# Kernel tuning notes

Hardware: AMD Instinct MI355X
Metric: run time of the kernel (lower is better)

The kernel has to match this reference:

```python
import jax, jax.numpy as jnp
import numpy as np

B, L, H = 1, 2048, 2048          # batch, seq_len, hidden_size
E, N, K, R = 4096, 16, 4, 128    # intermediate, ssm_state, conv_kernel, dt_rank


def setup_inputs() -> dict:
    key = jax.random.key(0)
    ks = jax.random.split(key, 8)
    s = 0.02
    inp = {
        "hidden_states": jax.random.normal(ks[0], (B, L, H), jnp.float32),
        "in_proj_w": jax.random.normal(ks[1], (2 * E, H), jnp.float32) * s,
        "conv_w": jax.random.normal(ks[2], (E, 1, K), jnp.float32) * s,
        "conv_b": jax.random.normal(ks[3], (E,), jnp.float32) * s,
        "x_proj_w": jax.random.normal(ks[4], (R + 2 * N, E), jnp.float32) * s,
        "dt_proj_w": jax.random.normal(ks[5], (E, R), jnp.float32) * s,
        "dt_proj_b": jax.random.normal(ks[6], (E,), jnp.float32) * s,
        "A_log": jnp.broadcast_to(jnp.log(jnp.arange(1, N + 1, dtype=jnp.float32))[None, :], (E, N)).copy(),
        "D": jnp.ones((E,), jnp.float32),
        "out_proj_w": jax.random.normal(ks[7], (H, E), jnp.float32) * s,
    }
    return inp


def _mamba_mixer(hidden_states, in_proj_w, conv_w, conv_b, x_proj_w,
                 dt_proj_w, dt_proj_b, A_log, D, out_proj_w):
    # in_proj -> [B, L, 2E], split into hidden / gate
    proj = jnp.einsum('blh,eh->ble', hidden_states, in_proj_w)
    h, gate = jnp.split(proj, 2, axis=-1)            # each [B, L, E]

    # depthwise causal conv1d over time, padding K-1 on the left
    h_c = h.transpose(0, 2, 1)                       # [B, E, L]
    h_c = jax.lax.conv_general_dilated(
        h_c, conv_w, window_strides=(1,), padding=[(K - 1, 0)],
        feature_group_count=E, dimension_numbers=('NCH', 'OIH', 'NCH'))
    h_c = h_c + conv_b[None, :, None]
    h = jax.nn.silu(h_c).transpose(0, 2, 1)          # [B, L, E]

    # x_proj -> dt, B, C (input-dependent SSM params)
    ssm = jnp.einsum('ble,pe->blp', h, x_proj_w)     # [B, L, R+2N]
    dt, Bp, Cp = jnp.split(ssm, [R, R + N], axis=-1)
    dt = jax.nn.softplus(jnp.einsum('blr,er->ble', dt, dt_proj_w) + dt_proj_b)  # [B,L,E]

    A = -jnp.exp(A_log)                              # [E, N]
    dA = jnp.exp(dt[..., None] * A)                  # [B, L, E, N]
    dBu = (dt * h)[..., None] * Bp[:, :, None, :]    # [B, L, E, N]

    # selective scan: s_t = dA_t * s_{t-1} + dBu_t
    def step(s, xs):
        dA_t, dBu_t = xs
        s = s * dA_t + dBu_t
        return s, s

    s0 = jnp.zeros((h.shape[0], E, N), h.dtype)
    _, states = jax.lax.scan(step, s0, (dA.transpose(1, 0, 2, 3), dBu.transpose(1, 0, 2, 3)))
    # states: [L, B, E, N]
    y = jnp.einsum('lben,bln->ble', states, Cp)      # [B, L, E]
    y = y + h * D                                    # skip via D
    y = y * jax.nn.silu(gate)                        # gated output
    return jnp.einsum('ble,he->blh', y, out_proj_w)  # [B, L, H]


def reference(hidden_states, in_proj_w, conv_w, conv_b, x_proj_w,
              dt_proj_w, dt_proj_b, A_log, D, out_proj_w):
    return _mamba_mixer(hidden_states, in_proj_w, conv_w, conv_b, x_proj_w,
                        dt_proj_w, dt_proj_b, A_log, D, out_proj_w)
```

## Files before the change

kernel.cpp:

```cpp
#include <hip/hip_runtime.h>

#define LL 2048
#define HH 2048
#define EE 4096
#define NS 16
#define RR 128
#define CT 32
#define NC (LL / CT)
#define BM 128
#define BN 128
#define BK 64

typedef __bf16 bf16x8 __attribute__((ext_vector_type(8)));
typedef float f32x4 __attribute__((ext_vector_type(4)));

__device__ __forceinline__ unsigned short f2bf(float f) {
  union { float f; unsigned int u; } v; v.f = f;
  unsigned int r = v.u + 0x7fffu + ((v.u >> 16) & 1u);
  return (unsigned short)(r >> 16);
}

__device__ __forceinline__ float bf2f(unsigned short u) {
  union { unsigned int i; float f; } v;
  v.i = ((unsigned int)u) << 16;
  return v.f;
}

__device__ __forceinline__ float softplus_fast(float x) {
  if (x > 20.0f) return x;
  float e = __builtin_amdgcn_exp2f(1.44269504f * x);
  return 0.69314718f * __builtin_amdgcn_logf(1.0f + e);
}

__device__ __forceinline__ void async_cp16(const unsigned short* g,
                                           unsigned short* l) {
  __builtin_amdgcn_global_load_lds(
      (const __attribute__((address_space(1))) unsigned int*)g,
      (__attribute__((address_space(3))) unsigned int*)l, 16, 0, 0);
}

#define P_C0 (LL * HH / 4)
#define P_C1 (P_C0 + 2 * EE * HH / 4)
#define P_C2 (P_C1 + 160 * EE / 4)
#define P_C3 (P_C2 + EE * RR / 4)
#define P_C4 (P_C3 + HH * EE / 4)
#define P_C5 (P_C4 + LL * 160 / 4)
#define P_C6 (P_C5 + LL * HH / 4)

__global__ __launch_bounds__(256) void prep_k(
    const float* __restrict__ hs, unsigned short* __restrict__ hsb,
    const float* __restrict__ w1, unsigned short* __restrict__ w1b,
    const float* __restrict__ xw, unsigned short* __restrict__ xwb,
    const float* __restrict__ dtw, unsigned short* __restrict__ dtwb,
    const float* __restrict__ ow, unsigned short* __restrict__ owb,
    float* __restrict__ ssm, float* __restrict__ out) {
  int i = blockIdx.x * 256 + threadIdx.x;
  const float* src = nullptr;
  unsigned short* dst = nullptr;
  int k = 0;
  if (i < P_C0)      { src = hs;  dst = hsb;  k = i; }
  else if (i < P_C1) { src = w1;  dst = w1b;  k = i - P_C0; }
  else if (i < P_C2) { src = xw;  dst = xwb;  k = i - P_C1; }
  else if (i < P_C3) { src = dtw; dst = dtwb; k = i - P_C2; }
  else if (i < P_C4) { src = ow;  dst = owb;  k = i - P_C3; }
  else if (i < P_C5) {
    float4 z; z.x = z.y = z.z = z.w = 0.0f;
    reinterpret_cast<float4*>(ssm)[i - P_C4] = z;
    return;
  } else {
    float4 z; z.x = z.y = z.z = z.w = 0.0f;
    reinterpret_cast<float4*>(out)[i - P_C5] = z;
    return;
  }
  float4 v = reinterpret_cast<const float4*>(src)[k];
  ushort4 o;
  o.x = f2bf(v.x); o.y = f2bf(v.y); o.z = f2bf(v.z); o.w = f2bf(v.w);
  reinterpret_cast<ushort4*>(dst)[k] = o;
}

template <int EPI>
__global__ __launch_bounds__(512, 2) void gemm256(
    const unsigned short* __restrict__ A,
    const unsigned short* __restrict__ B,
    float* __restrict__ C,
    int M, int N, int K, int tilesM, int splitk,
    float* __restrict__ auxF, unsigned short* __restrict__ auxB) {
  __shared__ __align__(16) unsigned short As[2][16384];
  __shared__ __align__(16) unsigned short Bs[2][16384];

  int bid = blockIdx.x;
  int tnInner = bid & 7;
  int rest = bid >> 3;
  int tm = rest % tilesM;
  int tn = (rest / tilesM) * 8 + tnInner;

  int Kslice = K / splitk;
  int k_begin = blockIdx.y * Kslice;
  int NT = Kslice / 64;

  int tid = threadIdx.x;
  int lane = tid & 63;
  int wave = tid >> 6;
  int wm = wave >> 2;
  int wn = wave & 3;
  int m16 = lane & 15, quad = lane >> 4;

  const unsigned short* Ab = A + (size_t)tm * 256 * K;
  const unsigned short* Bb = B + (size_t)tn * 256 * K;

  int rowS = tid >> 3;
  int gcbS = (tid & 7) ^ (rowS & 7);
  int ldsWB = (tid & ~63) * 8;

  int sw = m16 & 7;
  int coff0 = (quad ^ sw) << 3;
  int coff1 = ((4 + quad) ^ sw) << 3;
  int aoff = (wm * 128 + m16) * 64;
  int boff = (wn * 64 + m16) * 64;

  f32x4 acc[8][4];
#pragma unroll
  for (int i = 0; i < 8; ++i)
#pragma unroll
    for (int j = 0; j < 4; ++j)
#pragma unroll
      for (int t = 0; t < 4; ++t) acc[i][j][t] = 0.0f;

  auto stageA = [&](int bufb, int t, int h) {
    int kt = k_begin + t * 64;
    unsigned short* dst = &As[bufb][0];
#pragma unroll
    for (int c = 2 * h; c < 2 * h + 2; ++c)
      async_cp16(Ab + (size_t)(c * 64 + rowS) * K + kt + gcbS * 8,
                 dst + c * 4096 + ldsWB);
  };
  auto stageB = [&](int bufb, int t, int h) {
    int kt = k_begin + t * 64;
    unsigned short* dst = &Bs[bufb][0];
#pragma unroll
    for (int c = 2 * h; c < 2 * h + 2; ++c)
      async_cp16(Bb + (size_t)(c * 64 + rowS) * K + kt + gcbS * 8,
                 dst + c * 4096 + ldsWB);
  };

  stageA(0, 0, 0); stageA(0, 0, 1);
  stageB(0, 0, 0); stageB(0, 0, 1);
  stageB(1, 1, 0); stageB(1, 1, 1);
  stageA(1, 1, 0);
  asm volatile("s_waitcnt vmcnt(6)" ::: "memory");
  __builtin_amdgcn_s_barrier();

  bf16x8 a[4][2], b0[2][2], b1[2][2];

  for (int t0 = 0; t0 < NT; t0 += 2) {
    int t1 = t0 + 1;
    bool notLast = (t0 + 2 < NT);
    unsigned short* A0 = &As[0][0];
    unsigned short* B0 = &Bs[0][0];
    unsigned short* A1 = &As[1][0];
    unsigned short* B1 = &Bs[1][0];

#pragma unroll
    for (int i = 0; i < 4; ++i) {
      a[i][0] = *reinterpret_cast<const bf16x8*>(&A0[aoff + i * 1024 + coff0]);
      a[i][1] = *reinterpret_cast<const bf16x8*>(&A0[aoff + i * 1024 + coff1]);
    }
#pragma unroll
    for (int j = 0; j < 2; ++j) {
      b0[j][0] = *reinterpret_cast<const bf16x8*>(&B0[boff + j * 1024 + coff0]);
      b0[j][1] = *reinterpret_cast<const bf16x8*>(&B0[boff + j * 1024 + coff1]);
    }
    stageA(1, t1, 1);
    __builtin_amdgcn_s_barrier();
    asm volatile("s_waitcnt lgkmcnt(0)" ::: "memory");
    __builtin_amdgcn_sched_barrier(0);
    __builtin_amdgcn_s_setprio(1);
#pragma unroll
    for (int kk = 0; kk < 2; ++kk)
#pragma unroll
      for (int i = 0; i < 4; ++i)
#pragma unroll
        for (int j = 0; j < 2; ++j)
          acc[i][j] = __builtin_amdgcn_mfma_f32_16x16x32_bf16(
              a[i][kk], b0[j][kk], acc[i][j], 0, 0, 0);
    __builtin_amdgcn_s_setprio(0);
    __builtin_amdgcn_s_barrier();

#pragma unroll
    for (int j = 0; j < 2; ++j) {
      b1[j][0] = *reinterpret_cast<const bf16x8*>(&B0[boff + (2 + j) * 1024 + coff0]);
      b1[j][1] = *reinterpret_cast<const bf16x8*>(&B0[boff + (2 + j) * 1024 + coff1]);
    }
    __builtin_amdgcn_s_barrier();
    asm volatile("s_waitcnt lgkmcnt(0)" ::: "memory");
    __builtin_amdgcn_sched_barrier(0);
    __builtin_amdgcn_s_setprio(1);
#pragma unroll
    for (int kk = 0; kk < 2; ++kk)
#pragma unroll
      for (int i = 0; i < 4; ++i)
#pragma unroll
        for (int j = 0; j < 2; ++j)
          acc[i][2 + j] = __builtin_amdgcn_mfma_f32_16x16x32_bf16(
              a[i][kk], b1[j][kk], acc[i][2 + j], 0, 0, 0);
    __builtin_amdgcn_s_setprio(0);
    __builtin_amdgcn_s_barrier();

#pragma unroll
    for (int i = 0; i < 4; ++i) {
      a[i][0] = *reinterpret_cast<const bf16x8*>(&A0[aoff + (4 + i) * 1024 + coff0]);
      a[i][1] = *reinterpret_cast<const bf16x8*>(&A0[aoff + (4 + i) * 1024 + coff1]);
    }
    if (notLast) stageB(0, t0 + 2, 0);
    __builtin_amdgcn_s_barrier();
    asm volatile("s_waitcnt lgkmcnt(0)" ::: "memory");
    __builtin_amdgcn_sched_barrier(0);
    __builtin_amdgcn_s_setprio(1);
#pragma unroll
    for (int kk = 0; kk < 2; ++kk)
#pragma unroll
      for (int i = 0; i < 4; ++i)
#pragma unroll
        for (int j = 0; j < 2; ++j)
          acc[4 + i][2 + j] = __builtin_amdgcn_mfma_f32_16x16x32_bf16(
              a[i][kk], b1[j][kk], acc[4 + i][2 + j], 0, 0, 0);
    __builtin_amdgcn_s_setprio(0);
    __builtin_amdgcn_s_barrier();

    if (notLast) stageB(0, t0 + 2, 1);
    __builtin_amdgcn_s_setprio(1);
#pragma unroll
    for (int kk = 0; kk < 2; ++kk)
#pragma unroll
      for (int i = 0; i < 4; ++i)
#pragma unroll
        for (int j = 0; j < 2; ++j)
          acc[4 + i][j] = __builtin_amdgcn_mfma_f32_16x16x32_bf16(
              a[i][kk], b0[j][kk], acc[4 + i][j], 0, 0, 0);
    __builtin_amdgcn_s_setprio(0);
    if (notLast) {
      asm volatile("s_waitcnt vmcnt(4)" ::: "memory");
    } else {
      asm volatile("s_waitcnt vmcnt(0)" ::: "memory");
    }
    __builtin_amdgcn_s_barrier();

#pragma unroll
    for (int i = 0; i < 4; ++i) {
      a[i][0] = *reinterpret_cast<const bf16x8*>(&A1[aoff + i * 1024 + coff0]);
      a[i][1] = *reinterpret_cast<const bf16x8*>(&A1[aoff + i * 1024 + coff1]);
    }
#pragma unroll
    for (int j = 0; j < 2; ++j) {
      b0[j][0] = *reinterpret_cast<const bf16x8*>(&B1[boff + j * 1024 + coff0]);
      b0[j][1] = *reinterpret_cast<const bf16x8*>(&B1[boff + j * 1024 + coff1]);
    }
    if (notLast) stageA(0, t0 + 2, 0);
    __builtin_amdgcn_s_barrier();
    asm volatile("s_waitcnt lgkmcnt(0)" ::: "memory");
    __builtin_amdgcn_sched_barrier(0);
    __builtin_amdgcn_s_setprio(1);
#pragma unroll
    for (int kk = 0; kk < 2; ++kk)
#pragma unroll
      for (int i = 0; i < 4; ++i)
#pragma unroll
        for (int j = 0; j < 2; ++j)
          acc[i][j] = __builtin_amdgcn_mfma_f32_16x16x32_bf16(
              a[i][kk], b0[j][kk], acc[i][j], 0, 0, 0);
    __builtin_amdgcn_s_setprio(0);
    __builtin_amdgcn_s_barrier();

#pragma unroll
    for (int j = 0; j < 2; ++j) {
      b1[j][0] = *reinterpret_cast<const bf16x8*>(&B1[boff + (2 + j) * 1024 + coff0]);
      b1[j][1] = *reinterpret_cast<const bf16x8*>(&B1[boff + (2 + j) * 1024 + coff1]);
    }
    if (notLast) stageA(0, t0 + 2, 1);
    __builtin_amdgcn_s_barrier();
    asm volatile("s_waitcnt lgkmcnt(0)" ::: "memory");
    __builtin_amdgcn_sched_barrier(0);
    __builtin_amdgcn_s_setprio(1);
#pragma unroll
    for (int kk = 0; kk < 2; ++kk)
#pragma unroll
      for (int i = 0; i < 4; ++i)
#pragma unroll
        for (int j = 0; j < 2; ++j)
          acc[i][2 + j] = __builtin_amdgcn_mfma_f32_16x16x32_bf16(
              a[i][kk], b1[j][kk], acc[i][2 + j], 0, 0, 0);
    __builtin_amdgcn_s_setprio(0);
    __builtin_amdgcn_s_barrier();

#pragma unroll
    for (int i = 0; i < 4; ++i) {
      a[i][0] = *reinterpret_cast<const bf16x8*>(&A1[aoff + (4 + i) * 1024 + coff0]);
      a[i][1] = *reinterpret_cast<const bf16x8*>(&A1[aoff + (4 + i) * 1024 + coff1]);
    }
    if (notLast) stageB(1, t1 + 2, 0);
    __builtin_amdgcn_s_barrier();
    asm volatile("s_waitcnt lgkmcnt(0)" ::: "memory");
    __builtin_amdgcn_sched_barrier(0);
    __builtin_amdgcn_s_setprio(1);
#pragma unroll
    for (int kk = 0; kk < 2; ++kk)
#pragma unroll
      for (int i = 0; i < 4; ++i)
#pragma unroll
        for (int j = 0; j < 2; ++j)
          acc[4 + i][2 + j] = __builtin_amdgcn_mfma_f32_16x16x32_bf16(
              a[i][kk], b1[j][kk], acc[4 + i][2 + j], 0, 0, 0);
    __builtin_amdgcn_s_setprio(0);
    __builtin_amdgcn_s_barrier();

    if (notLast) { stageB(1, t1 + 2, 1); stageA(1, t1 + 2, 0); }
    __builtin_amdgcn_s_setprio(1);
#pragma unroll
    for (int kk = 0; kk < 2; ++kk)
#pragma unroll
      for (int i = 0; i < 4; ++i)
#pragma unroll
        for (int j = 0; j < 2; ++j)
          acc[4 + i][j] = __builtin_amdgcn_mfma_f32_16x16x32_bf16(
              a[i][kk], b0[j][kk], acc[4 + i][j], 0, 0, 0);
    __builtin_amdgcn_s_setprio(0);
    if (notLast) {
      asm volatile("s_waitcnt vmcnt(6)" ::: "memory");
    }
    __builtin_amdgcn_s_barrier();
  }

  int rowB = tm * 256 + wm * 128;
  int colB = tn * 256 + wn * 64;
  if constexpr (EPI == 1) {
#pragma unroll
    for (int mi = 0; mi < 8; ++mi)
#pragma unroll
      for (int nj = 0; nj < 4; ++nj) {
        int col = colB + nj * 16 + m16;
        int row0 = rowB + mi * 16 + quad * 4;
#pragma unroll
        for (int t4 = 0; t4 < 4; ++t4)
          atomicAdd(&C[(size_t)(row0 + t4) * N + col], acc[mi][nj][t4]);
      }
  } else {
    if (colB < EE) {
#pragma unroll
      for (int mi = 0; mi < 8; ++mi)
#pragma unroll
        for (int nj = 0; nj < 4; ++nj) {
          int col = colB + nj * 16 + m16;
          int row0 = rowB + mi * 16 + quad * 4;
#pragma unroll
          for (int t4 = 0; t4 < 4; ++t4)
            auxF[(size_t)(row0 + t4) * EE + col] = acc[mi][nj][t4];
        }
    } else {
#pragma unroll
      for (int mi = 0; mi < 8; ++mi)
#pragma unroll
        for (int nj = 0; nj < 4; ++nj) {
          int cg = colB + nj * 16 + m16 - EE;
          int row0 = rowB + mi * 16 + quad * 4;
#pragma unroll
          for (int t4 = 0; t4 < 4; ++t4) {
            float v = acc[mi][nj][t4];
            float s = v / (1.0f + __expf(-v));
            auxB[(size_t)(row0 + t4) * EE + cg] = f2bf(s);
          }
        }
    }
  }
}

template <int EPI>
__global__ __launch_bounds__(256) void gemm_lds_t(
    const unsigned short* __restrict__ A,
    const unsigned short* __restrict__ B,
    float* __restrict__ C,
    int M, int N, int K, int tilesM, int splitk,
    const float* __restrict__ bias, float* __restrict__ auxF,
    unsigned short* __restrict__ auxB) {
  __shared__ __align__(16) unsigned short As[BM * BK];
  __shared__ __align__(16) unsigned short Bs[BN * BK];

  int bid = blockIdx.x;
  int tnInner = bid & 7;
  int rest = bid >> 3;
  int tm = rest % tilesM;
  int tnOuter = rest / tilesM;
  int tn = tnOuter * 8 + tnInner;

  int Kslice = K / splitk;
  int k_begin = blockIdx.y * Kslice;
  int k_end = k_begin + Kslice;

  int tid = threadIdx.x;
  int lane = tid & 63;
  int wave = tid >> 6;
  int wm = wave & 1, wn = wave >> 1;
  int m16 = lane & 15, quad = lane >> 4;

  const unsigned short* Ab = A + (size_t)tm * BM * K;
  const unsigned short* Bb = B + (size_t)tn * BN * K;

  int srow[4], sgcb[4];
#pragma unroll
  for (int it = 0; it < 4; ++it) {
    int blk = it * 256 + tid;
    srow[it] = blk >> 3;
    sgcb[it] = (blk & 7) ^ (srow[it] & 7);
  }
  int ldsbase = (tid & ~63) * 8;

  f32x4 acc[4][4];
#pragma unroll
  for (int i = 0; i < 4; ++i)
#pragma unroll
    for (int j = 0; j < 4; ++j)
#pragma unroll
      for (int t = 0; t < 4; ++t) acc[i][j][t] = 0.0f;

  for (int k0 = k_begin; k0 < k_end; k0 += BK) {
    __syncthreads();
#pragma unroll
    for (int it = 0; it < 4; ++it)
      async_cp16(Ab + (size_t)srow[it] * K + k0 + sgcb[it] * 8,
                 &As[it * 2048 + ldsbase]);
#pragma unroll
    for (int it = 0; it < 4; ++it)
      async_cp16(Bb + (size_t)srow[it] * K + k0 + sgcb[it] * 8,
                 &Bs[it * 2048 + ldsbase]);
    __syncthreads();
#pragma unroll
    for (int kk = 0; kk < 2; ++kk) {
      bf16x8 a[4], b[4];
#pragma unroll
      for (int i = 0; i < 4; ++i) {
        int rr = wm * 64 + i * 16 + m16;
        int cb = (kk << 2) + quad;
        a[i] = *reinterpret_cast<const bf16x8*>(
            &As[rr * BK + ((cb ^ (rr & 7)) << 3)]);
      }
#pragma unroll
      for (int j = 0; j < 4; ++j) {
        int rr = wn * 64 + j * 16 + m16;
        int cb = (kk << 2) + quad;
        b[j] = *reinterpret_cast<const bf16x8*>(
            &Bs[rr * BK + ((cb ^ (rr & 7)) << 3)]);
      }
#pragma unroll
      for (int i = 0; i < 4; ++i)
#pragma unroll
        for (int j = 0; j < 4; ++j)
          acc[i][j] =
              __builtin_amdgcn_mfma_f32_16x16x32_bf16(a[i], b[j], acc[i][j], 0, 0, 0);
    }
  }

  int rowB = tm * BM + wm * 64;
  int colB = tn * BN + wn * 64;
  if constexpr (EPI == 1) {
#pragma unroll
    for (int i = 0; i < 4; ++i)
#pragma unroll
      for (int j = 0; j < 4; ++j) {
        int col = colB + j * 16 + m16;
        int row0 = rowB + i * 16 + quad * 4;
#pragma unroll
        for (int t = 0; t < 4; ++t)
          atomicAdd(&C[(size_t)(row0 + t) * N + col], acc[i][j][t]);
      }
  } else {
#pragma unroll
    for (int i = 0; i < 4; ++i)
#pragma unroll
      for (int j = 0; j < 4; ++j) {
        int col = colB + j * 16 + m16;
        float bv = bias[col];
        int row0 = rowB + i * 16 + quad * 4;
#pragma unroll
        for (int t = 0; t < 4; ++t) {
          float x = acc[i][j][t] + bv;
          auxB[(size_t)(row0 + t) * EE + col] = f2bf(softplus_fast(x));
        }
      }
  }
}

__global__ __launch_bounds__(256) void gemm_bt(
    const unsigned short* __restrict__ A,
    const unsigned short* __restrict__ B,
    float* __restrict__ C,
    int M, int N, int K, int tilesN, int splitk) {
  int bid = blockIdx.x;
  int groupSize = 8 * tilesN;
  int g = bid / groupSize, r = bid % groupSize;
  int tm = g * 8 + (r & 7);
  int tn = r >> 3;

  int Kslice = K / splitk;
  int k_begin = blockIdx.y * Kslice;
  int k_end = k_begin + Kslice;

  int tid = threadIdx.x;
  int wave = tid >> 6, lane = tid & 63;
  int wm = wave & 1, wn = wave >> 1;
  int m16 = lane & 15, quad = lane >> 4;
  int rowBase = tm * 64 + wm * 32;
  int colBase = tn * 128 + wn * 64;

  const unsigned short* a0p = A + (size_t)(rowBase + m16) * K + quad * 8;
  const unsigned short* a1p = A + (size_t)(rowBase + 16 + m16) * K + quad * 8;
  const unsigned short* bp[4];
  bool bok[4];
#pragma unroll
  for (int j = 0; j < 4; ++j) {
    int col = colBase + j * 16 + m16;
    bok[j] = (col < N);
    bp[j] = B + (size_t)(bok[j] ? col : 0) * K + quad * 8;
  }

  f32x4 acc[2][4];
#pragma unroll
  for (int i = 0; i < 2; ++i)
#pragma unroll
    for (int j = 0; j < 4; ++j)
#pragma unroll
      for (int t = 0; t < 4; ++t) acc[i][j][t] = 0.0f;

  bf16x8 zero8;
#pragma unroll
  for (int t = 0; t < 8; ++t) zero8[t] = (__bf16)0.0f;

  for (int k = k_begin; k < k_end; k += 32) {
    bf16x8 a0 = *reinterpret_cast<const bf16x8*>(a0p + k);
    bf16x8 a1 = *reinterpret_cast<const bf16x8*>(a1p + k);
    bf16x8 b[4];
#pragma unroll
    for (int j = 0; j < 4; ++j)
      b[j] = bok[j] ? *reinterpret_cast<const bf16x8*>(bp[j] + k) : zero8;
#pragma unroll
    for (int j = 0; j < 4; ++j) {
      acc[0][j] = __builtin_amdgcn_mfma_f32_16x16x32_bf16(a0, b[j], acc[0][j], 0, 0, 0);
      acc[1][j] = __builtin_amdgcn_mfma_f32_16x16x32_bf16(a1, b[j], acc[1][j], 0, 0, 0);
    }
  }

#pragma unroll
  for (int i = 0; i < 2; ++i)
#pragma unroll
    for (int j = 0; j < 4; ++j) {
      int col = colBase + j * 16 + m16;
      if (col >= N) continue;
      int row0 = rowBase + i * 16 + quad * 4;
      if (splitk == 1) {
#pragma unroll
        for (int t = 0; t < 4; ++t)
          C[(size_t)(row0 + t) * N + col] = acc[i][j][t];
      } else {
#pragma unroll
        for (int t = 0; t < 4; ++t)
          atomicAdd(&C[(size_t)(row0 + t) * N + col], acc[i][j][t]);
      }
    }
}

__global__ __launch_bounds__(256) void conv_silu_k(
    const float* __restrict__ projh, const float* __restrict__ cw,
    const float* __restrict__ cb, unsigned short* __restrict__ hb) {
  int e = blockIdx.x * 256 + threadIdx.x;
  int l0 = blockIdx.y * 16;
  float w0 = cw[e * 4 + 0], w1 = cw[e * 4 + 1];
  float w2 = cw[e * 4 + 2], w3 = cw[e * 4 + 3];
  float bias = cb[e];
  float xm3 = (l0 >= 3) ? projh[(size_t)(l0 - 3) * EE + e] : 0.0f;
  float xm2 = (l0 >= 2) ? projh[(size_t)(l0 - 2) * EE + e] : 0.0f;
  float xm1 = (l0 >= 1) ? projh[(size_t)(l0 - 1) * EE + e] : 0.0f;
#pragma unroll
  for (int t = 0; t < 16; ++t) {
    int l = l0 + t;
    float x0 = projh[(size_t)l * EE + e];
    float acc = bias + w0 * xm3 + w1 * xm2 + w2 * xm1 + w3 * x0;
    float s = acc / (1.0f + __expf(-acc));
    hb[(size_t)l * EE + e] = f2bf(s);
    xm3 = xm2; xm2 = xm1; xm1 = x0;
  }
}

__global__ void dtcast_k(const float* __restrict__ ssm,
                         unsigned short* __restrict__ dtin, int n) {
  int i = blockIdx.x * blockDim.x + threadIdx.x;
  if (i >= n) return;
  int l = i >> 7, r = i & 127;
  dtin[i] = f2bf(ssm[l * 160 + r]);
}

__global__ __launch_bounds__(256) void scan_partA(
    const unsigned short* __restrict__ dtb, const unsigned short* __restrict__ hb,
    const float* __restrict__ ssm, const float* __restrict__ A_log,
    float* __restrict__ P, float* __restrict__ S) {
  int e = blockIdx.y * 256 + threadIdx.x;
  int c = blockIdx.x;
  float Aa[16];
#pragma unroll
  for (int q = 0; q < 4; ++q) {
    float4 a = reinterpret_cast<const float4*>(&A_log[(size_t)e * NS])[q];
    Aa[q * 4 + 0] = -__expf(a.x) * 1.44269504f;
    Aa[q * 4 + 1] = -__expf(a.y) * 1.44269504f;
    Aa[q * 4 + 2] = -__expf(a.z) * 1.44269504f;
    Aa[q * 4 + 3] = -__expf(a.w) * 1.44269504f;
  }
  float s[16], p[16];
#pragma unroll
  for (int n = 0; n < 16; ++n) { s[n] = 0.0f; p[n] = 1.0f; }
  int l0 = c * CT;
#pragma unroll 2
  for (int t = 0; t < CT; ++t) {
    int l = l0 + t;
    size_t o = (size_t)l * EE + e;
    float dtv = bf2f(dtb[o]);
    float hv = bf2f(hb[o]);
    float Bv[16];
#pragma unroll
    for (int q = 0; q < 4; ++q)
      *reinterpret_cast<float4*>(&Bv[q * 4]) =
          reinterpret_cast<const float4*>(&ssm[(size_t)l * 160 + 128])[q];
    float z = dtv * hv;
#pragma unroll
    for (int n = 0; n < 16; ++n) {
      float dA = __builtin_amdgcn_exp2f(dtv * Aa[n]);
      s[n] = s[n] * dA + z * Bv[n];
      p[n] *= dA;
    }
  }
  size_t base = ((size_t)c * EE + e) * NS;
#pragma unroll
  for (int q = 0; q < 4; ++q) {
    reinterpret_cast<float4*>(&P[base])[q] = *reinterpret_cast<float4*>(&p[q * 4]);
    reinterpret_cast<float4*>(&S[base])[q] = *reinterpret_cast<float4*>(&s[q * 4]);
  }
}

__global__ __launch_bounds__(256) void scan_chunkB(
    const float* __restrict__ P, float* __restrict__ S) {
  int gidx = blockIdx.x * 256 + threadIdx.x;
  float s = 0.0f;
  float pv = P[gidx], sv = S[gidx];
  for (int c = 0; c < NC; ++c) {
    float pn = 0.0f, sn = 0.0f;
    if (c + 1 < NC) {
      size_t i2 = (size_t)(c + 1) * (EE * NS) + gidx;
      pn = P[i2];
      sn = S[i2];
    }
    float s_next = s * pv + sv;
    S[(size_t)c * (EE * NS) + gidx] = s;
    s = s_next;
    pv = pn; sv = sn;
  }
}

__global__ __launch_bounds__(256) void scan_partC(
    const unsigned short* __restrict__ dtb, const unsigned short* __restrict__ hb,
    const float* __restrict__ ssm, const float* __restrict__ A_log,
    const float* __restrict__ Dp, const unsigned short* __restrict__ sg,
    const float* __restrict__ Sinit, unsigned short* __restrict__ yb) {
  int e = blockIdx.y * 256 + threadIdx.x;
  int c = blockIdx.x;
  float Aa[16];
#pragma unroll
  for (int q = 0; q < 4; ++q) {
    float4 a = reinterpret_cast<const float4*>(&A_log[(size_t)e * NS])[q];
    Aa[q * 4 + 0] = -__expf(a.x) * 1.44269504f;
    Aa[q * 4 + 1] = -__expf(a.y) * 1.44269504f;
    Aa[q * 4 + 2] = -__expf(a.z) * 1.44269504f;
    Aa[q * 4 + 3] = -__expf(a.w) * 1.44269504f;
  }
  float Dv = Dp[e];
  float s[16];
  size_t base = ((size_t)c * EE + e) * NS;
#pragma unroll
  for (int q = 0; q < 4; ++q)
    *reinterpret_cast<float4*>(&s[q * 4]) =
        reinterpret_cast<const float4*>(&Sinit[base])[q];
  int l0 = c * CT;
#pragma unroll 2
  for (int t = 0; t < CT; ++t) {
    int l = l0 + t;
    size_t o = (size_t)l * EE + e;
    float dtv = bf2f(dtb[o]);
    float hv = bf2f(hb[o]);
    float Bv[16], Cv[16];
#pragma unroll
    for (int q = 0; q < 4; ++q) {
      *reinterpret_cast<float4*>(&Bv[q * 4]) =
          reinterpret_cast<const float4*>(&ssm[(size_t)l * 160 + 128])[q];
      *reinterpret_cast<float4*>(&Cv[q * 4]) =
          reinterpret_cast<const float4*>(&ssm[(size_t)l * 160 + 144])[q];
    }
    float z = dtv * hv;
    float y = 0.0f;
#pragma unroll
    for (int n = 0; n < 16; ++n) {
      float dA = __builtin_amdgcn_exp2f(dtv * Aa[n]);
      s[n] = s[n] * dA + z * Bv[n];
      y += s[n] * Cv[n];
    }
    float gv = bf2f(sg[o]);
    float yv = (y + hv * Dv) * gv;
    yb[o] = f2bf(yv);
  }
}

extern "C" void kernel_launch(void* const* d_in, const int* in_sizes, int n_in,
                              void* d_out, int out_size, void* d_ws, size_t ws_size,
                              hipStream_t stream) {
  const float* hs   = (const float*)d_in[0];
  const float* w1   = (const float*)d_in[1];
  const float* cw   = (const float*)d_in[2];
  const float* cb   = (const float*)d_in[3];
  const float* xw   = (const float*)d_in[4];
  const float* dtw  = (const float*)d_in[5];
  const float* dtb  = (const float*)d_in[6];
  const float* Alog = (const float*)d_in[7];
  const float* Dp   = (const float*)d_in[8];
  const float* ow   = (const float*)d_in[9];
  float* out = (float*)d_out;

  char* ws = (char*)d_ws;
  size_t off = 0;
  auto alloc = [&](size_t b) {
    char* p = ws + off;
    off += (b + 255) & ~(size_t)255;
    return p;
  };
  float* projh = (float*)alloc((size_t)LL * EE * 4);
  unsigned short* sg  = (unsigned short*)alloc((size_t)LL * EE * 2);
  unsigned short* hb  = (unsigned short*)alloc((size_t)LL * EE * 2);
  unsigned short* dtb_buf = (unsigned short*)alloc((size_t)LL * EE * 2);
  unsigned short* w1b = (unsigned short*)alloc((size_t)2 * EE * HH * 2);
  unsigned short* hsb = (unsigned short*)alloc((size_t)LL * HH * 2);
  unsigned short* yb  = (unsigned short*)alloc((size_t)LL * EE * 2);
  unsigned short* owb = (unsigned short*)alloc((size_t)HH * EE * 2);
  unsigned short* xwb = (unsigned short*)alloc((size_t)160 * EE * 2);
  float* ssm = (float*)alloc((size_t)LL * 160 * 4);
  unsigned short* dtin = (unsigned short*)alloc((size_t)LL * RR * 2);
  unsigned short* dtwb = (unsigned short*)alloc((size_t)EE * RR * 2);
  float* Pbuf = (float*)alloc((size_t)NC * EE * NS * 4);
  float* Sbuf = (float*)alloc((size_t)NC * EE * NS * 4);

  prep_k<<<P_C6 / 256, 256, 0, stream>>>(hs, hsb, w1, w1b, xw, xwb, dtw, dtwb,
                                         ow, owb, ssm, out);

  {
    int tilesM = LL / 256;
    int tilesN = (2 * EE) / 256;
    gemm256<2><<<dim3(tilesM * tilesN, 1), 512, 0, stream>>>(
        hsb, w1b, nullptr, LL, 2 * EE, HH, tilesM, 1, projh, sg);
  }
  conv_silu_k<<<dim3(EE / 256, LL / 16), 256, 0, stream>>>(projh, cw, cb, hb);
  {
    int tilesN = (160 + 127) / 128, tilesM = LL / 64;
    gemm_bt<<<dim3(tilesM * tilesN, 8), 256, 0, stream>>>(
        hb, xwb, ssm, LL, 160, EE, tilesN, 8);
  }
  dtcast_k<<<(LL * RR + 255) / 256, 256, 0, stream>>>(ssm, dtin, LL * RR);
  {
    int tilesN = EE / BN, tilesM = LL / BM;
    gemm_lds_t<4><<<dim3(tilesM * tilesN, 1), 256, 0, stream>>>(
        dtin, dtwb, nullptr, LL, EE, RR, tilesM, 1, dtb, nullptr, dtb_buf);
  }
  scan_partA<<<dim3(NC, EE / 256), 256, 0, stream>>>(dtb_buf, hb, ssm, Alog,
                                                     Pbuf, Sbuf);
  scan_chunkB<<<EE * NS / 256, 256, 0, stream>>>(Pbuf, Sbuf);
  scan_partC<<<dim3(NC, EE / 256), 256, 0, stream>>>(dtb_buf, hb, ssm, Alog, Dp,
                                                     sg, Sbuf, yb);
  {
    int tilesN = HH / BN, tilesM = LL / BM;
    gemm_lds_t<1><<<dim3(tilesM * tilesN, 2), 256, 0, stream>>>(
        yb, owb, out, LL, HH, EE, tilesM, 2, nullptr, nullptr, nullptr);
  }
}
```

Baseline: 416.2 us.

## Replace split-K out_proj GEMM with double-buffered async-LDS 128x128 kernel

New measurement: 393.0 us. -5.6%, faster.

```diff
diff --git a/kernel.cpp b/kernel.cpp
--- a/kernel.cpp
+++ b/kernel.cpp
@@ -45,7 +45,6 @@
 #define P_C3 (P_C2 + EE * RR / 4)
 #define P_C4 (P_C3 + HH * EE / 4)
 #define P_C5 (P_C4 + LL * 160 / 4)
-#define P_C6 (P_C5 + LL * HH / 4)
 
 __global__ __launch_bounds__(256) void prep_k(
     const float* __restrict__ hs, unsigned short* __restrict__ hsb,
@@ -53,7 +52,7 @@
     const float* __restrict__ xw, unsigned short* __restrict__ xwb,
     const float* __restrict__ dtw, unsigned short* __restrict__ dtwb,
     const float* __restrict__ ow, unsigned short* __restrict__ owb,
-    float* __restrict__ ssm, float* __restrict__ out) {
+    float* __restrict__ ssm) {
   int i = blockIdx.x * 256 + threadIdx.x;
   const float* src = nullptr;
   unsigned short* dst = nullptr;
@@ -63,13 +62,9 @@
   else if (i < P_C2) { src = xw;  dst = xwb;  k = i - P_C1; }
   else if (i < P_C3) { src = dtw; dst = dtwb; k = i - P_C2; }
   else if (i < P_C4) { src = ow;  dst = owb;  k = i - P_C3; }
-  else if (i < P_C5) {
+  else {
     float4 z; z.x = z.y = z.z = z.w = 0.0f;
     reinterpret_cast<float4*>(ssm)[i - P_C4] = z;
-    return;
-  } else {
-    float4 z; z.x = z.y = z.z = z.w = 0.0f;
-    reinterpret_cast<float4*>(out)[i - P_C5] = z;
     return;
   }
   float4 v = reinterpret_cast<const float4*>(src)[k];
@@ -371,6 +366,268 @@
         }
     }
   }
+}
+
+__global__ __launch_bounds__(256, 2) void gemm128p(
+    const unsigned short* __restrict__ A,
+    const unsigned short* __restrict__ B,
+    float* __restrict__ C,
+    int M, int N, int K, int tilesM) {
+  __shared__ __align__(16) unsigned short As[2][8192];
+  __shared__ __align__(16) unsigned short Bs[2][8192];
+
+  int bid = blockIdx.x;
+  int tnInner = bid & 7;
+  int rest = bid >> 3;
+  int tm = rest % tilesM;
+  int tn = (rest / tilesM) * 8 + tnInner;
+
+  int NT = K / 64;
+
+  int tid = threadIdx.x;
+  int lane = tid & 63;
+  int wave = tid >> 6;
+  int wm = wave >> 1;
+  int wn = wave & 1;
+  int m16 = lane & 15, quad = lane >> 4;
+
+  const unsigned short* Ab = A + (size_t)tm * 128 * K;
+  const unsigned short* Bb = B + (size_t)tn * 128 * K;
+
+  int rowS = tid >> 3;
+  int gcbS = (tid & 7) ^ (rowS & 7);
+  int ldsWB = (tid & ~63) * 8;
+
+  int sw = m16 & 7;
+  int coff0 = (quad ^ sw) << 3;
+  int coff1 = ((4 + quad) ^ sw) << 3;
+  int aoff = (wm * 64 + m16) * 64;
+  int boff = (wn * 64 + m16) * 64;
+
+  f32x4 acc[4][4];
+#pragma unroll
+  for (int i = 0; i < 4; ++i)
+#pragma unroll
+    for (int j = 0; j < 4; ++j)
+#pragma unroll
+      for (int t = 0; t < 4; ++t) acc[i][j][t] = 0.0f;
+
+  auto stageA = [&](int bufb, int t, int h) {
+    int kt = t * 64;
+    unsigned short* dst = &As[bufb][0];
+#pragma unroll
+    for (int c = 2 * h; c < 2 * h + 2; ++c)
+      async_cp16(Ab + (size_t)(c * 32 + rowS) * K + kt + gcbS * 8,
+                 dst + c * 2048 + ldsWB);
+  };
+  auto stageB = [&](int bufb, int t, int h) {
+    int kt = t * 64;
+    unsigned short* dst = &Bs[bufb][0];
+#pragma unroll
+    for (int c = 2 * h; c < 2 * h + 2; ++c)
+      async_cp16(Bb + (size_t)(c * 32 + rowS) * K + kt + gcbS * 8,
+                 dst + c * 2048 + ldsWB);
+  };
+
+  stageA(0, 0, 0); stageA(0, 0, 1);
+  stageB(0, 0, 0); stageB(0, 0, 1);
+  stageB(1, 1, 0); stageB(1, 1, 1);
+  stageA(1, 1, 0);
+  asm volatile("s_waitcnt vmcnt(6)" ::: "memory");
+  __builtin_amdgcn_s_barrier();
+
+  bf16x8 a[2][2], b0[2][2], b1[2][2];
+
+  for (int t0 = 0; t0 < NT; t0 += 2) {
+    int t1 = t0 + 1;
+    bool notLast = (t0 + 2 < NT);
+    unsigned short* A0 = &As[0][0];
+    unsigned short* B0 = &Bs[0][0];
+    unsigned short* A1 = &As[1][0];
+    unsigned short* B1 = &Bs[1][0];
+
+#pragma unroll
+    for (int i = 0; i < 2; ++i) {
+      a[i][0] = *reinterpret_cast<const bf16x8*>(&A0[aoff + i * 1024 + coff0]);
+      a[i][1] = *reinterpret_cast<const bf16x8*>(&A0[aoff + i * 1024 + coff1]);
+    }
+#pragma unroll
+    for (int j = 0; j < 2; ++j) {
+      b0[j][0] = *reinterpret_cast<const bf16x8*>(&B0[boff + j * 1024 + coff0]);
+      b0[j][1] = *reinterpret_cast<const bf16x8*>(&B0[boff + j * 1024 + coff1]);
+    }
+    stageA(1, t1, 1);
+    __builtin_amdgcn_s_barrier();
+    asm volatile("s_waitcnt lgkmcnt(0)" ::: "memory");
+    __builtin_amdgcn_sched_barrier(0);
+    __builtin_amdgcn_s_setprio(1);
+#pragma unroll
+    for (int kk = 0; kk < 2; ++kk)
+#pragma unroll
+      for (int i = 0; i < 2; ++i)
+#pragma unroll
+        for (int j = 0; j < 2; ++j)
+          acc[i][j] = __builtin_amdgcn_mfma_f32_16x16x32_bf16(
+              a[i][kk], b0[j][kk], acc[i][j], 0, 0, 0);
+    __builtin_amdgcn_s_setprio(0);
+    __builtin_amdgcn_s_barrier();
+
+#pragma unroll
+    for (int j = 0; j < 2; ++j) {
+      b1[j][0] = *reinterpret_cast<const bf16x8*>(&B0[boff + (2 + j) * 1024 + coff0]);
+      b1[j][1] = *reinterpret_cast<const bf16x8*>(&B0[boff + (2 + j) * 1024 + coff1]);
+    }
+    __builtin_amdgcn_s_barrier();
+    asm volatile("s_waitcnt lgkmcnt(0)" ::: "memory");
+    __builtin_amdgcn_sched_barrier(0);
+    __builtin_amdgcn_s_setprio(1);
+#pragma unroll
+    for (int kk = 0; kk < 2; ++kk)
+#pragma unroll
+      for (int i = 0; i < 2; ++i)
+#pragma unroll
+        for (int j = 0; j < 2; ++j)
+          acc[i][2 + j] = __builtin_amdgcn_mfma_f32_16x16x32_bf16(
+              a[i][kk], b1[j][kk], acc[i][2 + j], 0, 0, 0);
+    __builtin_amdgcn_s_setprio(0);
+    __builtin_amdgcn_s_barrier();
+
+#pragma unroll
+    for (int i = 0; i < 2; ++i) {
+      a[i][0] = *reinterpret_cast<const bf16x8*>(&A0[aoff + (2 + i) * 1024 + coff0]);
+      a[i][1] = *reinterpret_cast<const bf16x8*>(&A0[aoff + (2 + i) * 1024 + coff1]);
+    }
+    if (notLast) stageB(0, t0 + 2, 0);
+    __builtin_amdgcn_s_barrier();
+    asm volatile("s_waitcnt lgkmcnt(0)" ::: "memory");
+    __builtin_amdgcn_sched_barrier(0);
+    __builtin_amdgcn_s_setprio(1);
+#pragma unroll
+    for (int kk = 0; kk < 2; ++kk)
+#pragma unroll
+      for (int i = 0; i < 2; ++i)
+#pragma unroll
+        for (int j = 0; j < 2; ++j)
+          acc[2 + i][2 + j] = __builtin_amdgcn_mfma_f32_16x16x32_bf16(
+              a[i][kk], b1[j][kk], acc[2 + i][2 + j], 0, 0, 0);
+    __builtin_amdgcn_s_setprio(0);
+    __builtin_amdgcn_s_barrier();
+
+    if (notLast) stageB(0, t0 + 2, 1);
+    __builtin_amdgcn_s_setprio(1);
+#pragma unroll
+    for (int kk = 0; kk < 2; ++kk)
+#pragma unroll
+      for (int i = 0; i < 2; ++i)
+#pragma unroll
+        for (int j = 0; j < 2; ++j)
+          acc[2 + i][j] = __builtin_amdgcn_mfma_f32_16x16x32_bf16(
+              a[i][kk], b0[j][kk], acc[2 + i][j], 0, 0, 0);
+    __builtin_amdgcn_s_setprio(0);
+    if (notLast) {
+      asm volatile("s_waitcnt vmcnt(4)" ::: "memory");
+    } else {
+      asm volatile("s_waitcnt vmcnt(0)" ::: "memory");
+    }
+    __builtin_amdgcn_s_barrier();
+
+#pragma unroll
+    for (int i = 0; i < 2; ++i) {
+      a[i][0] = *reinterpret_cast<const bf16x8*>(&A1[aoff + i * 1024 + coff0]);
+      a[i][1] = *reinterpret_cast<const bf16x8*>(&A1[aoff + i * 1024 + coff1]);
+    }
+#pragma unroll
+    for (int j = 0; j < 2; ++j) {
+      b0[j][0] = *reinterpret_cast<const bf16x8*>(&B1[boff + j * 1024 + coff0]);
+      b0[j][1] = *reinterpret_cast<const bf16x8*>(&B1[boff + j * 1024 + coff1]);
+    }
+    if (notLast) stageA(0, t0 + 2, 0);
+    __builtin_amdgcn_s_barrier();
+    asm volatile("s_waitcnt lgkmcnt(0)" ::: "memory");
+    __builtin_amdgcn_sched_barrier(0);
+    __builtin_amdgcn_s_setprio(1);
+#pragma unroll
+    for (int kk = 0; kk < 2; ++kk)
+#pragma unroll
+      for (int i = 0; i < 2; ++i)
+#pragma unroll
+        for (int j = 0; j < 2; ++j)
+          acc[i][j] = __builtin_amdgcn_mfma_f32_16x16x32_bf16(
+              a[i][kk], b0[j][kk], acc[i][j], 0, 0, 0);
+    __builtin_amdgcn_s_setprio(0);
+    __builtin_amdgcn_s_barrier();
+
+#pragma unroll
+    for (int j = 0; j < 2; ++j) {
+      b1[j][0] = *reinterpret_cast<const bf16x8*>(&B1[boff + (2 + j) * 1024 + coff0]);
+      b1[j][1] = *reinterpret_cast<const bf16x8*>(&B1[boff + (2 + j) * 1024 + coff1]);
+    }
+    if (notLast) stageA(0, t0 + 2, 1);
+    __builtin_amdgcn_s_barrier();
+    asm volatile("s_waitcnt lgkmcnt(0)" ::: "memory");
+    __builtin_amdgcn_sched_barrier(0);
+    __builtin_amdgcn_s_setprio(1);
+#pragma unroll
+    for (int kk = 0; kk < 2; ++kk)
+#pragma unroll
+      for (int i = 0; i < 2; ++i)
+#pragma unroll
+        for (int j = 0; j < 2; ++j)
+          acc[i][2 + j] = __builtin_amdgcn_mfma_f32_16x16x32_bf16(
+              a[i][kk], b1[j][kk], acc[i][2 + j], 0, 0, 0);
+    __builtin_amdgcn_s_setprio(0);
+    __builtin_amdgcn_s_barrier();
+
+#pragma unroll
+    for (int i = 0; i < 2; ++i) {
+      a[i][0] = *reinterpret_cast<const bf16x8*>(&A1[aoff + (2 + i) * 1024 + coff0]);
+      a[i][1] = *reinterpret_cast<const bf16x8*>(&A1[aoff + (2 + i) * 1024 + coff1]);
+    }
+    if (notLast) stageB(1, t1 + 2, 0);
+    __builtin_amdgcn_s_barrier();
+    asm volatile("s_waitcnt lgkmcnt(0)" ::: "memory");
+    __builtin_amdgcn_sched_barrier(0);
+    __builtin_amdgcn_s_setprio(1);
+#pragma unroll
+    for (int kk = 0; kk < 2; ++kk)
+#pragma unroll
+      for (int i = 0; i < 2; ++i)
+#pragma unroll
+        for (int j = 0; j < 2; ++j)
+          acc[2 + i][2 + j] = __builtin_amdgcn_mfma_f32_16x16x32_bf16(
+              a[i][kk], b1[j][kk], acc[2 + i][2 + j], 0, 0, 0);
+    __builtin_amdgcn_s_setprio(0);
+    __builtin_amdgcn_s_barrier();
+
+    if (notLast) { stageB(1, t1 + 2, 1); stageA(1, t1 + 2, 0); }
+    __builtin_amdgcn_s_setprio(1);
+#pragma unroll
+    for (int kk = 0; kk < 2; ++kk)
+#pragma unroll
+      for (int i = 0; i < 2; ++i)
+#pragma unroll
+        for (int j = 0; j < 2; ++j)
+          acc[2 + i][j] = __builtin_amdgcn_mfma_f32_16x16x32_bf16(
+              a[i][kk], b0[j][kk], acc[2 + i][j], 0, 0, 0);
+    __builtin_amdgcn_s_setprio(0);
+    if (notLast) {
+      asm volatile("s_waitcnt vmcnt(6)" ::: "memory");
+    }
+    __builtin_amdgcn_s_barrier();
+  }
+
+  int rowB = tm * 128 + wm * 64;
+  int colB = tn * 128 + wn * 64;
+#pragma unroll
+  for (int mi = 0; mi < 4; ++mi)
+#pragma unroll
+    for (int nj = 0; nj < 4; ++nj) {
+      int col = colB + nj * 16 + m16;
+      int row0 = rowB + mi * 16 + quad * 4;
+#pragma unroll
+      for (int t4 = 0; t4 < 4; ++t4)
+        C[(size_t)(row0 + t4) * N + col] = acc[mi][nj][t4];
+    }
 }
 
 template <int EPI>
@@ -750,8 +1007,8 @@
   float* Pbuf = (float*)alloc((size_t)NC * EE * NS * 4);
   float* Sbuf = (float*)alloc((size_t)NC * EE * NS * 4);
 
-  prep_k<<<P_C6 / 256, 256, 0, stream>>>(hs, hsb, w1, w1b, xw, xwb, dtw, dtwb,
-                                         ow, owb, ssm, out);
+  prep_k<<<P_C5 / 256, 256, 0, stream>>>(hs, hsb, w1, w1b, xw, xwb, dtw, dtwb,
+                                         ow, owb, ssm);
 
   {
     int tilesM = LL / 256;
@@ -777,8 +1034,8 @@
   scan_partC<<<dim3(NC, EE / 256), 256, 0, stream>>>(dtb_buf, hb, ssm, Alog, Dp,
                                                      sg, Sbuf, yb);
   {
-    int tilesN = HH / BN, tilesM = LL / BM;
-    gemm_lds_t<1><<<dim3(tilesM * tilesN, 2), 256, 0, stream>>>(
-        yb, owb, out, LL, HH, EE, tilesM, 2, nullptr, nullptr, nullptr);
-  }
-}
+    int tilesM = LL / 128, tilesN = HH / 128;
+    gemm128p<<<dim3(tilesM * tilesN, 1), 256, 0, stream>>>(
+        yb, owb, out, LL, HH, EE, tilesM);
+  }
+}
```
